# Optimization experiments

Measured on AMD Instinct MI355X. Metric: run time of the kernel, lower is better.

The kernel has to match this reference:

```python
import jax, jax.numpy as jnp
import numpy as np

N, IN_DIM, OUT_DIM, E = 50000, 64, 64, 800000


def setup_inputs() -> dict:
    key = jax.random.key(0)
    k1, k2, k3, k4 = jax.random.split(key, 4)
    x = jax.random.normal(k1, (N, IN_DIM), dtype=jnp.float32)
    edge_index = jax.random.randint(k2, (2, E), 0, N, dtype=jnp.int64)
    # nn.Linear(in_dim, out_dim): weight [out, in], bias [out]
    bound = 1.0 / np.sqrt(IN_DIM)
    W = jax.random.uniform(k3, (OUT_DIM, IN_DIM), minval=-bound, maxval=bound, dtype=jnp.float32)
    b = jax.random.uniform(k4, (OUT_DIM,), minval=-bound, maxval=bound, dtype=jnp.float32)
    return {"x": x, "edge_index": edge_index, "W": W, "b": b}


def reference(x, edge_index, W, b):
    row, col = edge_index[0], edge_index[1]
    n = x.shape[0]
    # deg = bincount(row, minlength=N) + 1e-6, shape [N, 1]
    deg = jnp.zeros((n,), dtype=jnp.float32).at[row].add(1.0)[:, None] + 1e-6
    # agg[row] += x[col]  (gather + scatter-add)
    agg = jnp.zeros_like(x).at[row].add(x[col])
    agg = agg / deg
    return agg @ W.T + b
```

## Files before the change

### kernel.cpp

```cpp
#include <hip/hip_runtime.h>
#include <hip/hip_bf16.h>

#define N_NODES 50000
#define DIM 64
#define N_EDGES 800000
#define CAP 64
#define NTHR 256
#define GB_ROWS 32
#define SLICE 6250
#define NGROUP 196
#define TOTAL_BLOCKS (NGROUP * 24)
#define CHUNK_EDGES 2048


typedef __attribute__((ext_vector_type(8))) short bf16x8;
typedef __attribute__((ext_vector_type(4))) float f32x4;

static __device__ inline unsigned int f2bf(float f) {
    __hip_bfloat16 h = __float2bfloat16(f);
    return (unsigned int)*reinterpret_cast<unsigned short*>(&h);
}
static __device__ inline float bf_lo(unsigned int u) { return __uint_as_float(u << 16); }
static __device__ inline float bf_hi(unsigned int u) { return __uint_as_float(u & 0xffff0000u); }

__global__ __launch_bounds__(NTHR) void init_kernel(
    const float* __restrict__ W, int* __restrict__ count,
    uint4* __restrict__ wpk)
{
    int t = threadIdx.x, b = blockIdx.x;
    if (b < 196) {
        int i = b * NTHR + t;
        if (i < N_NODES) count[i] = 0;
    } else {
        for (int i = t; i < 512; i += NTHR) {
            int n = i >> 3, kg = i & 7;
            const float* wr = W + n * DIM + kg * 8;
            uint4 uw;
            uw.x = f2bf(wr[0]) | (f2bf(wr[1]) << 16);
            uw.y = f2bf(wr[2]) | (f2bf(wr[3]) << 16);
            uw.z = f2bf(wr[4]) | (f2bf(wr[5]) << 16);
            uw.w = f2bf(wr[6]) | (f2bf(wr[7]) << 16);
            wpk[(n << 3) | (kg ^ (n & 7))] = uw;
        }
    }
}

__global__ __launch_bounds__(NTHR, 8) void place_gemm_kernel(
    const int* __restrict__ ei, const float* __restrict__ x,
    const uint4* __restrict__ wpk, int* __restrict__ count,
    unsigned short* __restrict__ csr16, unsigned short* __restrict__ yb)
{
    __shared__ float4 xs4[GB_ROWS * 16];
    __shared__ uint4  Wb[512];

    int t = threadIdx.x;
    int b = blockIdx.x;
    int m = b % 24;

    if (m < 8) {
        int g  = (b / 24) * 8 + m;
        int R0 = g * GB_ROWS;
        if (R0 < N_NODES) {
            const float4* x4 = (const float4*)x;
            for (int i = t; i < GB_ROWS * 16; i += NTHR) {
                int r = i >> 4, c = i & 15;
                int q = (R0 + r) * 16 + c;
                float4 v = (q < N_NODES * 16) ? x4[q]
                                              : make_float4(0.f, 0.f, 0.f, 0.f);
                xs4[(r << 4) | (c ^ (r & 15))] = v;
            }
            for (int i = t; i < 512; i += NTHR)
                Wb[i] = wpk[i];
            __syncthreads();

            int w  = t >> 6, l = t & 63;
            int rt = w >> 1, ch = w & 1;
            int lm = l & 15, lg = l >> 4;
            int mloc = rt * 16 + lm;

            f32x4 acc0 = {0.f, 0.f, 0.f, 0.f};
            f32x4 acc1 = {0.f, 0.f, 0.f, 0.f};
#pragma unroll
            for (int kc = 0; kc < 2; kc++) {
                int c0 = kc * 8 + lg * 2;
                float4 xa = xs4[(mloc << 4) | ((c0    ) ^ lm)];
                float4 xb = xs4[(mloc << 4) | ((c0 + 1) ^ lm)];
                float xv[8] = {xa.x, xa.y, xa.z, xa.w, xb.x, xb.y, xb.z, xb.w};
                bf16x8 ahi, alo;
#pragma unroll
                for (int j = 0; j < 8; j++) {
                    unsigned hb = f2bf(xv[j]);
                    float lo = xv[j] - __uint_as_float(hb << 16);
                    ahi[j] = (short)hb;
                    alo[j] = (short)f2bf(lo);
                }
                int kgg = kc * 4 + lg;
#pragma unroll
                for (int ctl = 0; ctl < 2; ctl++) {
                    int n = (ch * 2 + ctl) * 16 + lm;
                    uint4 wq = Wb[(n << 3) | (kgg ^ (n & 7))];
                    bf16x8 bfr = *reinterpret_cast<bf16x8*>(&wq);
                    if (ctl == 0) {
                        acc0 = __builtin_amdgcn_mfma_f32_16x16x32_bf16(ahi, bfr, acc0, 0, 0, 0);
                        acc0 = __builtin_amdgcn_mfma_f32_16x16x32_bf16(alo, bfr, acc0, 0, 0, 0);
                    } else {
                        acc1 = __builtin_amdgcn_mfma_f32_16x16x32_bf16(ahi, bfr, acc1, 0, 0, 0);
                        acc1 = __builtin_amdgcn_mfma_f32_16x16x32_bf16(alo, bfr, acc1, 0, 0, 0);
                    }
                }
            }
#pragma unroll
            for (int ctl = 0; ctl < 2; ctl++) {
                f32x4 acc = ctl ? acc1 : acc0;
                int n = (ch * 2 + ctl) * 16 + lm;
#pragma unroll
                for (int q = 0; q < 4; q++) {
                    int rr = R0 + rt * 16 + lg * 4 + q;
                    if (rr < N_NODES)
                        yb[(size_t)rr * DIM + n] = (unsigned short)f2bf(acc[q]);
                }
            }
        }
    } else {
        int s    = b & 7;
        int lo   = s * SLICE;
        int q    = (b / 24) * 2 + ((m - 8) >> 3);
        int e0   = q * CHUNK_EDGES + t * 8;
        if (e0 < N_EDGES) {
            const int4* rp = (const int4*)(ei + e0);
            int4 ra = rp[0];
            int4 rb = rp[1];
            int rows[8] = {ra.x, ra.y, ra.z, ra.w, rb.x, rb.y, rb.z, rb.w};
#pragma unroll
            for (int k = 0; k < 8; k++) {
                if ((unsigned)(rows[k] - lo) < (unsigned)SLICE) {
                    int col = ei[N_EDGES + e0 + k];
                    int pos = atomicAdd(&count[rows[k]], 1);
                    if (pos < CAP)
                        csr16[rows[k] * CAP + pos] = (unsigned short)col;
                }
            }
        }
    }
}

__global__ __launch_bounds__(NTHR) void agg_kernel(
    const unsigned short* __restrict__ yb, const int* __restrict__ count,
    const unsigned short* __restrict__ csr16, const float* __restrict__ bias,
    float* __restrict__ out)
{
    int t   = threadIdx.x;
    int w   = t >> 6;
    int l   = t & 63;
    int sub = l & 7;
    int grp = l >> 3;
    int sb  = blockIdx.x & 7;
    int i   = blockIdx.x >> 3;
    int rl  = i * 4 + w;
    if (rl >= SLICE) return;
    int r = sb * SLICE + rl;

    int deg = count[r];
    int dc  = deg < CAP ? deg : CAP;
    int myc = csr16[(size_t)r * CAP + l];

    const uint4* ybq = (const uint4*)yb;
    float s[8];
#pragma unroll
    for (int q = 0; q < 8; q++) s[q] = 0.f;

    bool valid = grp < dc;
    {
        int c0 = __shfl(myc, grp);
        int cs = valid ? c0 : 0;
        uint4 v = ybq[(size_t)cs * 8 + sub];
        for (int jb = 8; jb < dc; jb += 8) {
            int  j2     = jb + grp;
            int  c2     = __shfl(myc, j2);
            bool valid2 = j2 < dc;
            int  cs2    = valid2 ? c2 : 0;
            uint4 v2 = ybq[(size_t)cs2 * 8 + sub];
            if (valid) {
                s[0] += bf_lo(v.x); s[1] += bf_hi(v.x);
                s[2] += bf_lo(v.y); s[3] += bf_hi(v.y);
                s[4] += bf_lo(v.z); s[5] += bf_hi(v.z);
                s[6] += bf_lo(v.w); s[7] += bf_hi(v.w);
            }
            v = v2; valid = valid2;
        }
        if (valid) {
            s[0] += bf_lo(v.x); s[1] += bf_hi(v.x);
            s[2] += bf_lo(v.y); s[3] += bf_hi(v.y);
            s[4] += bf_lo(v.z); s[5] += bf_hi(v.z);
            s[6] += bf_lo(v.w); s[7] += bf_hi(v.w);
        }
    }
#pragma unroll
    for (int q = 0; q < 8; q++) {
        s[q] += __shfl_xor(s[q], 8);
        s[q] += __shfl_xor(s[q], 16);
        s[q] += __shfl_xor(s[q], 32);
    }

    if (grp == 0) {
        float inv_d = 1.0f / ((float)deg + 1e-6f);
        float4 b0 = ((const float4*)bias)[2 * sub];
        float4 b1 = ((const float4*)bias)[2 * sub + 1];
        float4 o0 = make_float4(s[0] * inv_d + b0.x, s[1] * inv_d + b0.y,
                                s[2] * inv_d + b0.z, s[3] * inv_d + b0.w);
        float4 o1 = make_float4(s[4] * inv_d + b1.x, s[5] * inv_d + b1.y,
                                s[6] * inv_d + b1.z, s[7] * inv_d + b1.w);
        ((float4*)(out + (size_t)r * DIM))[2 * sub]     = o0;
        ((float4*)(out + (size_t)r * DIM))[2 * sub + 1] = o1;
    }
}

extern "C" void kernel_launch(void* const* d_in, const int* in_sizes, int n_in,
                              void* d_out, int out_size, void* d_ws, size_t ws_size,
                              hipStream_t stream) {
    const float* x    = (const float*)d_in[0];
    const int*   ei   = (const int*)d_in[1];
    const float* W    = (const float*)d_in[2];
    const float* bias = (const float*)d_in[3];
    float* out = (float*)d_out;

    int*            count = (int*)d_ws;
    unsigned short* yb    = (unsigned short*)((char*)d_ws + 262144);
    uint4*          wpk   = (uint4*)((char*)d_ws + 6815744);
    unsigned short* csr16 = (unsigned short*)((char*)d_ws + 8388608);

    init_kernel<<<197, NTHR, 0, stream>>>(W, count, wpk);
    place_gemm_kernel<<<TOTAL_BLOCKS, NTHR, 0, stream>>>(ei, x, wpk, count, csr16, yb);
    agg_kernel<<<8 * 1563, NTHR, 0, stream>>>(yb, count, csr16, bias, out);
}
```

Measured before the change: 129.6 us.

## Pre-pack edge row/col into 32-bit words and drop LDS staging in GEMM

The init kernel gains extra blocks that pack each edge's row and column into one 32-bit word, 16 bits each. The placement phase of the fused kernel then reads that packed array instead of the two int arrays. Each of the 8 slice passes re-reads the edge rows, so this shrinks that repeated traffic and removes the dependent column load. The GEMM blocks no longer stage x and W through shared memory and load them directly from global memory. This adds a full pass over edge_index up front, and the packing only holds while node indices fit in 16 bits.

```diff
diff --git a/kernel.cpp b/kernel.cpp
--- a/kernel.cpp
+++ b/kernel.cpp
@@ -11,6 +11,7 @@
 #define NGROUP 196
 #define TOTAL_BLOCKS (NGROUP * 24)
 #define CHUNK_EDGES 2048
+#define PACK_BLOCKS 782
 
 
 typedef __attribute__((ext_vector_type(8))) short bf16x8;
@@ -24,14 +25,15 @@
 static __device__ inline float bf_hi(unsigned int u) { return __uint_as_float(u & 0xffff0000u); }
 
 __global__ __launch_bounds__(NTHR) void init_kernel(
-    const float* __restrict__ W, int* __restrict__ count,
-    uint4* __restrict__ wpk)
+    const float* __restrict__ W, const int* __restrict__ ei,
+    int* __restrict__ count, uint4* __restrict__ wpk,
+    unsigned int* __restrict__ pack)
 {
     int t = threadIdx.x, b = blockIdx.x;
     if (b < 196) {
         int i = b * NTHR + t;
         if (i < N_NODES) count[i] = 0;
-    } else {
+    } else if (b == 196) {
         for (int i = t; i < 512; i += NTHR) {
             int n = i >> 3, kg = i & 7;
             const float* wr = W + n * DIM + kg * 8;
@@ -42,17 +44,26 @@
             uw.w = f2bf(wr[6]) | (f2bf(wr[7]) << 16);
             wpk[(n << 3) | (kg ^ (n & 7))] = uw;
         }
+    } else {
+        int gid = (b - 197) * NTHR + t;
+        if (gid * 4 < N_EDGES) {
+            int4 r4 = ((const int4*)ei)[gid];
+            int4 c4 = ((const int4*)(ei + N_EDGES))[gid];
+            uint4 o;
+            o.x = (unsigned)r4.x | ((unsigned)c4.x << 16);
+            o.y = (unsigned)r4.y | ((unsigned)c4.y << 16);
+            o.z = (unsigned)r4.z | ((unsigned)c4.z << 16);
+            o.w = (unsigned)r4.w | ((unsigned)c4.w << 16);
+            ((uint4*)pack)[gid] = o;
+        }
     }
 }
 
 __global__ __launch_bounds__(NTHR, 8) void place_gemm_kernel(
-    const int* __restrict__ ei, const float* __restrict__ x,
+    const unsigned int* __restrict__ pack, const float* __restrict__ x,
     const uint4* __restrict__ wpk, int* __restrict__ count,
     unsigned short* __restrict__ csr16, unsigned short* __restrict__ yb)
 {
-    __shared__ float4 xs4[GB_ROWS * 16];
-    __shared__ uint4  Wb[512];
-
     int t = threadIdx.x;
     int b = blockIdx.x;
     int m = b % 24;
@@ -61,30 +72,19 @@
         int g  = (b / 24) * 8 + m;
         int R0 = g * GB_ROWS;
         if (R0 < N_NODES) {
-            const float4* x4 = (const float4*)x;
-            for (int i = t; i < GB_ROWS * 16; i += NTHR) {
-                int r = i >> 4, c = i & 15;
-                int q = (R0 + r) * 16 + c;
-                float4 v = (q < N_NODES * 16) ? x4[q]
-                                              : make_float4(0.f, 0.f, 0.f, 0.f);
-                xs4[(r << 4) | (c ^ (r & 15))] = v;
-            }
-            for (int i = t; i < 512; i += NTHR)
-                Wb[i] = wpk[i];
-            __syncthreads();
-
             int w  = t >> 6, l = t & 63;
             int rt = w >> 1, ch = w & 1;
             int lm = l & 15, lg = l >> 4;
-            int mloc = rt * 16 + lm;
+            int r  = R0 + rt * 16 + lm;
+            int rc = r < N_NODES ? r : 0;
+            const float4* xr = (const float4*)(x + (size_t)rc * DIM);
 
             f32x4 acc0 = {0.f, 0.f, 0.f, 0.f};
             f32x4 acc1 = {0.f, 0.f, 0.f, 0.f};
 #pragma unroll
             for (int kc = 0; kc < 2; kc++) {
-                int c0 = kc * 8 + lg * 2;
-                float4 xa = xs4[(mloc << 4) | ((c0    ) ^ lm)];
-                float4 xb = xs4[(mloc << 4) | ((c0 + 1) ^ lm)];
+                float4 xa = xr[kc * 8 + lg * 2];
+                float4 xb = xr[kc * 8 + lg * 2 + 1];
                 float xv[8] = {xa.x, xa.y, xa.z, xa.w, xb.x, xb.y, xb.z, xb.w};
                 bf16x8 ahi, alo;
 #pragma unroll
@@ -98,7 +98,7 @@
 #pragma unroll
                 for (int ctl = 0; ctl < 2; ctl++) {
                     int n = (ch * 2 + ctl) * 16 + lm;
-                    uint4 wq = Wb[(n << 3) | (kgg ^ (n & 7))];
+                    uint4 wq = wpk[(n << 3) | (kgg ^ (n & 7))];
                     bf16x8 bfr = *reinterpret_cast<bf16x8*>(&wq);
                     if (ctl == 0) {
                         acc0 = __builtin_amdgcn_mfma_f32_16x16x32_bf16(ahi, bfr, acc0, 0, 0, 0);
@@ -127,17 +127,18 @@
         int q    = (b / 24) * 2 + ((m - 8) >> 3);
         int e0   = q * CHUNK_EDGES + t * 8;
         if (e0 < N_EDGES) {
-            const int4* rp = (const int4*)(ei + e0);
-            int4 ra = rp[0];
-            int4 rb = rp[1];
-            int rows[8] = {ra.x, ra.y, ra.z, ra.w, rb.x, rb.y, rb.z, rb.w};
+            const uint4* pp = (const uint4*)(pack + e0);
+            uint4 pa = pp[0];
+            uint4 pb = pp[1];
+            unsigned pk[8] = {pa.x, pa.y, pa.z, pa.w, pb.x, pb.y, pb.z, pb.w};
 #pragma unroll
             for (int k = 0; k < 8; k++) {
-                if ((unsigned)(rows[k] - lo) < (unsigned)SLICE) {
-                    int col = ei[N_EDGES + e0 + k];
-                    int pos = atomicAdd(&count[rows[k]], 1);
+                int row = (int)(pk[k] & 0xffffu);
+                if ((unsigned)(row - lo) < (unsigned)SLICE) {
+                    int col = (int)(pk[k] >> 16);
+                    int pos = atomicAdd(&count[row], 1);
                     if (pos < CAP)
-                        csr16[rows[k] * CAP + pos] = (unsigned short)col;
+                        csr16[row * CAP + pos] = (unsigned short)col;
                 }
             }
         }
@@ -227,9 +228,10 @@
     int*            count = (int*)d_ws;
     unsigned short* yb    = (unsigned short*)((char*)d_ws + 262144);
     uint4*          wpk   = (uint4*)((char*)d_ws + 6815744);
-    unsigned short* csr16 = (unsigned short*)((char*)d_ws + 8388608);
-
-    init_kernel<<<197, NTHR, 0, stream>>>(W, count, wpk);
-    place_gemm_kernel<<<TOTAL_BLOCKS, NTHR, 0, stream>>>(ei, x, wpk, count, csr16, yb);
+    unsigned int*   pack  = (unsigned int*)((char*)d_ws + 8388608);
+    unsigned short* csr16 = (unsigned short*)((char*)d_ws + 12582912);
+
+    init_kernel<<<197 + PACK_BLOCKS, NTHR, 0, stream>>>(W, ei, count, wpk, pack);
+    place_gemm_kernel<<<TOTAL_BLOCKS, NTHR, 0, stream>>>(pack, x, wpk, count, csr16, yb);
     agg_kernel<<<8 * 1563, NTHR, 0, stream>>>(yb, count, csr16, bias, out);
 }
```

After: 128.3 us. Within noise of the previous version (-1.1%).
